# Kernel tuning notes

Measured on AMD Instinct MI355X. Metric: run time of the kernel, lower is better.

## Reference

```python
import jax, jax.numpy as jnp
import numpy as np

D_MODEL, N_HEADS, D_FF = 768, 12, 3072
B, T = 4, 2048
EPS = 1e-5


def setup_inputs() -> dict:
    key = jax.random.key(0)
    ks = jax.random.split(key, 12)
    s = 0.02
    inp = {
        'x': jax.random.normal(ks[0], (B, T, D_MODEL), jnp.float32),
        'mask': jnp.tril(jnp.ones((1, 1, T, T), jnp.bool_)),  # causal decoder mask
        'ln1_g': jnp.ones((D_MODEL,), jnp.float32),
        'ln1_b': jnp.zeros((D_MODEL,), jnp.float32),
        'Wq': jax.random.normal(ks[1], (D_MODEL, D_MODEL), jnp.float32) * s,
        'bq': jnp.zeros((D_MODEL,), jnp.float32),
        'Wk': jax.random.normal(ks[2], (D_MODEL, D_MODEL), jnp.float32) * s,
        'bk': jnp.zeros((D_MODEL,), jnp.float32),
        'Wv': jax.random.normal(ks[3], (D_MODEL, D_MODEL), jnp.float32) * s,
        'bv': jnp.zeros((D_MODEL,), jnp.float32),
        'Wo': jax.random.normal(ks[4], (D_MODEL, D_MODEL), jnp.float32) * s,
        'bo': jnp.zeros((D_MODEL,), jnp.float32),
        'ln2_g': jnp.ones((D_MODEL,), jnp.float32),
        'ln2_b': jnp.zeros((D_MODEL,), jnp.float32),
        'W1': jax.random.normal(ks[5], (D_MODEL, D_FF), jnp.float32) * s,
        'b1': jnp.zeros((D_FF,), jnp.float32),
        'W2': jax.random.normal(ks[6], (D_FF, D_MODEL), jnp.float32) * s,
        'b2': jnp.zeros((D_MODEL,), jnp.float32),
    }
    return inp


def _layer_norm(x, g, b):
    mu = jnp.mean(x, axis=-1, keepdims=True)
    var = jnp.mean(jnp.square(x - mu), axis=-1, keepdims=True)
    return (x - mu) * jax.lax.rsqrt(var + EPS) * g + b


def reference(x, mask, ln1_g, ln1_b, Wq, bq, Wk, bk, Wv, bv, Wo, bo,
              ln2_g, ln2_b, W1, b1, W2, b2):
    Bx, Tx, _ = x.shape
    d_k = D_MODEL // N_HEADS
    # --- attention sublayer (pre-norm) ---
    h = _layer_norm(x, ln1_g, ln1_b)
    q = (h @ Wq + bq).reshape(Bx, Tx, N_HEADS, d_k).transpose(0, 2, 1, 3)
    k = (h @ Wk + bk).reshape(Bx, Tx, N_HEADS, d_k).transpose(0, 2, 1, 3)
    v = (h @ Wv + bv).reshape(Bx, Tx, N_HEADS, d_k).transpose(0, 2, 1, 3)
    scores = jnp.einsum('bhqd,bhkd->bhqk', q, k) / jnp.sqrt(jnp.float32(d_k))
    scores = jnp.where(mask, scores, -jnp.inf)
    weights = jax.nn.softmax(scores, axis=-1)
    attn = jnp.einsum('bhqk,bhkd->bhqd', weights, v)
    attn = attn.transpose(0, 2, 1, 3).reshape(Bx, Tx, D_MODEL)
    x = x + (attn @ Wo + bo)
    # --- FFN sublayer (pre-norm) ---
    h = _layer_norm(x, ln2_g, ln2_b)
    h = jax.nn.gelu(h @ W1 + b1, approximate=False)
    return x + (h @ W2 + b2)
```

## Files before the change

### kernel.cpp

```cpp
#include <hip/hip_runtime.h>

#define DEV __device__ __forceinline__

typedef __attribute__((ext_vector_type(8))) short short8;
typedef __attribute__((ext_vector_type(4))) float f32x4;
typedef __attribute__((ext_vector_type(4))) unsigned int u32x4;
typedef __attribute__((ext_vector_type(2))) unsigned int u32x2;
typedef __attribute__((ext_vector_type(4))) unsigned short u16x4;

constexpr int Bc = 4, Tc = 2048, Dm = 768, Hh = 12, DK = 64, DFF = 3072;
constexpr int MT = Bc * Tc;

DEV unsigned short f2bf(float f) {
  unsigned int u = __float_as_uint(f);
  u += 0x7fff + ((u >> 16) & 1);
  return (unsigned short)(u >> 16);
}

DEV unsigned cvt_pk_bf16(float lo, float hi) {
  unsigned r;
  asm("v_cvt_pk_bf16_f32 %0, %1, %2" : "=v"(r) : "v"(lo), "v"(hi));
  return r;
}

DEV float gelu_fast(float v) {
  float y = 1.5957691216f * (v + 0.044715f * v * v * v);
  return v * (1.0f / (1.0f + __expf(-y)));
}

DEV void gload_lds16(const void* g, void* l) {
  __builtin_amdgcn_global_load_lds(
      (const __attribute__((address_space(1))) void*)g,
      (__attribute__((address_space(3))) void*)l, 16, 0, 0);
}

__global__ __launch_bounds__(256) void ln_kernel(const float* __restrict__ x,
    const float* __restrict__ gam, const float* __restrict__ bet,
    unsigned short* __restrict__ out)
{
  int lane = threadIdx.x & 63;
  int row = blockIdx.x * 4 + (threadIdx.x >> 6);
  const float* xr = x + (size_t)row * Dm + lane * 12;
  f32x4 v0 = *(const f32x4*)(xr);
  f32x4 v1 = *(const f32x4*)(xr + 4);
  f32x4 v2 = *(const f32x4*)(xr + 8);
  float s = 0.f, s2 = 0.f;
#pragma unroll
  for (int j = 0; j < 4; j++) {
    s  += v0[j] + v1[j] + v2[j];
    s2 += v0[j]*v0[j] + v1[j]*v1[j] + v2[j]*v2[j];
  }
#pragma unroll
  for (int off = 32; off; off >>= 1) { s += __shfl_xor(s, off); s2 += __shfl_xor(s2, off); }
  float mu = s * (1.f / Dm);
  float inv = rsqrtf(s2 * (1.f / Dm) - mu * mu + 1e-5f);
  int cb = lane * 12;
  unsigned short o[12];
#pragma unroll
  for (int j = 0; j < 4; j++) {
    o[j]     = f2bf((v0[j] - mu) * inv * gam[cb + j]     + bet[cb + j]);
    o[4 + j] = f2bf((v1[j] - mu) * inv * gam[cb + 4 + j] + bet[cb + 4 + j]);
    o[8 + j] = f2bf((v2[j] - mu) * inv * gam[cb + 8 + j] + bet[cb + 8 + j]);
  }
  unsigned short* orow = out + (size_t)row * Dm + cb;
#pragma unroll
  for (int i = 0; i < 3; i++) *(u16x4*)(orow + i * 4) = *(const u16x4*)(&o[i * 4]);
}

__global__ __launch_bounds__(256) void wtrans_all_kernel(
    const float* __restrict__ Wq, const float* __restrict__ Wk,
    const float* __restrict__ Wv, const float* __restrict__ Wo,
    const float* __restrict__ W1, const float* __restrict__ W2,
    unsigned short* wq_t, unsigned short* wk_t, unsigned short* wv_t,
    unsigned short* wo_t, unsigned short* w1_t, unsigned short* w2_t)
{
  __shared__ unsigned short tile[32][33];
  int bid = blockIdx.x;
  const float* src; unsigned short* dst; int K, N, t;
  if (bid < 2304) {
    int w = bid / 576; t = bid % 576; K = Dm; N = Dm;
    src = w == 0 ? Wq : w == 1 ? Wk : w == 2 ? Wv : Wo;
    dst = w == 0 ? wq_t : w == 1 ? wk_t : w == 2 ? wv_t : wo_t;
  } else if (bid < 4608) {
    t = bid - 2304; K = Dm; N = DFF; src = W1; dst = w1_t;
  } else {
    t = bid - 4608; K = DFF; N = Dm; src = W2; dst = w2_t;
  }
  int gx = N / 32;
  int n0 = (t % gx) * 32, k0 = (t / gx) * 32;
  int tx = threadIdx.x & 31, ty = threadIdx.x >> 5;
#pragma unroll
  for (int i = 0; i < 4; i++) {
    int kr = ty * 4 + i;
    tile[kr][tx] = f2bf(src[(size_t)(k0 + kr) * N + n0 + tx]);
  }
  __syncthreads();
#pragma unroll
  for (int i = 0; i < 4; i++) {
    int nr = ty * 4 + i;
    dst[(size_t)(n0 + nr) * K + k0 + tx] = tile[tx][nr];
  }
}

template<int OUT_MODE, bool SWAP>
DEV void gemm_body(unsigned short* As, unsigned short* Bs,
    const unsigned short* __restrict__ A, const unsigned short* __restrict__ Bt,
    const float* __restrict__ bias, const float* __restrict__ resid, void* __restrict__ out,
    int M, int N, int K)
{
  int m0 = blockIdx.x * 128, n0 = blockIdx.y * 128;
  int tid = threadIdx.x, lane = tid & 63, wid = tid >> 6;
  int wr = wid >> 1, wc = wid & 1;
  int fr = lane & 15, fg = lane >> 4;
  f32x4 acc[4][4] = {};
  for (int k0 = 0; k0 < K; k0 += 64) {
    __syncthreads();
#pragma unroll
    for (int p = 0; p < 4; p++) {
      int L = wid * 256 + p * 64 + lane;
      int row = L >> 3, pos = L & 7;
      int ch = pos ^ (row & 7);
      gload_lds16(&A[(size_t)(m0 + row) * K + k0 + ch * 8],
                  &As[(size_t)(wid * 256 + p * 64) * 8]);
      gload_lds16(&Bt[(size_t)(n0 + row) * K + k0 + ch * 8],
                  &Bs[(size_t)(wid * 256 + p * 64) * 8]);
    }
    __syncthreads();
#pragma unroll
    for (int kk = 0; kk < 2; kk++) {
      short8 af[4], bfr[4];
#pragma unroll
      for (int m = 0; m < 4; m++) {
        int row = wr * 64 + m * 16 + fr;
        int ch = (kk * 4 + fg) ^ (fr & 7);
        af[m] = *(const short8*)(&As[row * 64 + ch * 8]);
      }
#pragma unroll
      for (int n = 0; n < 4; n++) {
        int row = wc * 64 + n * 16 + fr;
        int ch = (kk * 4 + fg) ^ (fr & 7);
        bfr[n] = *(const short8*)(&Bs[row * 64 + ch * 8]);
      }
#pragma unroll
      for (int m = 0; m < 4; m++)
#pragma unroll
        for (int n = 0; n < 4; n++) {
          if (SWAP)
            acc[m][n] = __builtin_amdgcn_mfma_f32_16x16x32_bf16(bfr[n], af[m], acc[m][n], 0, 0, 0);
          else
            acc[m][n] = __builtin_amdgcn_mfma_f32_16x16x32_bf16(af[m], bfr[n], acc[m][n], 0, 0, 0);
        }
    }
  }
  if (SWAP) {
#pragma unroll
    for (int m = 0; m < 4; m++) {
      int gm = m0 + wr * 64 + m * 16 + fr;
#pragma unroll
      for (int n = 0; n < 4; n++) {
        int gn0 = n0 + wc * 64 + n * 16 + fg * 4;
        f32x4 v = acc[m][n];
        f32x4 bv = *(const f32x4*)(bias + gn0);
#pragma unroll
        for (int rr = 0; rr < 4; rr++) v[rr] += bv[rr];
        if (OUT_MODE == 2) {
#pragma unroll
          for (int rr = 0; rr < 4; rr++) v[rr] = gelu_fast(v[rr]);
        }
        if (OUT_MODE == 0) {
          f32x4 rv = *(const f32x4*)(resid + (size_t)gm * N + gn0);
#pragma unroll
          for (int rr = 0; rr < 4; rr++) v[rr] += rv[rr];
          *(f32x4*)(&((float*)out)[(size_t)gm * N + gn0]) = v;
        } else {
          u32x2 pk;
          pk[0] = cvt_pk_bf16(v[0], v[1]);
          pk[1] = cvt_pk_bf16(v[2], v[3]);
          if (OUT_MODE == 3) {
            int b = gm >> 11, tt = gm & 2047, h = gn0 >> 6, d = gn0 & 63;
            *(u32x2*)(&((unsigned short*)out)[(((size_t)b * Hh + h) * Tc + tt) * DK + d]) = pk;
          } else {
            *(u32x2*)(&((unsigned short*)out)[(size_t)gm * N + gn0]) = pk;
          }
        }
      }
    }
  } else {
    int col = fr, rbase = fg * 4;
#pragma unroll
    for (int m = 0; m < 4; m++) {
#pragma unroll
      for (int n = 0; n < 4; n++) {
        int gn = n0 + wc * 64 + n * 16 + col;
        float bv = bias[gn];
        int gm0 = m0 + wr * 64 + m * 16 + rbase;
        int b = gm0 >> 11, tt = gm0 & 2047, h = gn >> 6, d = gn & 63;
        u16x4 pk;
#pragma unroll
        for (int rr = 0; rr < 4; rr++) pk[rr] = f2bf(acc[m][n][rr] + bv);
        *(u16x4*)(&((unsigned short*)out)[(((size_t)b * Hh + h) * DK + d) * Tc + tt]) = pk;
      }
    }
  }
}

__global__ __launch_bounds__(256) void gemm_f32out_kernel(const unsigned short* A,
    const unsigned short* Bt, const float* bias, const float* resid, float* out,
    int M, int N, int K)
{
  __shared__ unsigned short As[128 * 64], Bs[128 * 64];
  gemm_body<0, true>(As, Bs, A, Bt, bias, resid, out, M, N, K);
}

__global__ __launch_bounds__(256) void gemm_gelu_kernel(const unsigned short* A,
    const unsigned short* Bt, const float* bias, unsigned short* out,
    int M, int N, int K)
{
  __shared__ unsigned short As[128 * 64], Bs[128 * 64];
  gemm_body<2, true>(As, Bs, A, Bt, bias, nullptr, out, M, N, K);
}

__global__ __launch_bounds__(256) void gemm_qkv_kernel(const unsigned short* A,
    const unsigned short* Bq, const unsigned short* Bk, const unsigned short* Bv,
    const float* bq, const float* bk, const float* bv,
    unsigned short* oq, unsigned short* okh, unsigned short* ovt)
{
  __shared__ unsigned short As[128 * 64], Bs[128 * 64];
  if (blockIdx.z == 0)      gemm_body<1, true >(As, Bs, A, Bq, bq, nullptr, oq,  MT, Dm, Dm);
  else if (blockIdx.z == 1) gemm_body<3, true >(As, Bs, A, Bk, bk, nullptr, okh, MT, Dm, Dm);
  else                      gemm_body<4, false>(As, Bs, A, Bv, bv, nullptr, ovt, MT, Dm, Dm);
}

__global__ __launch_bounds__(256) void attn_kernel(const unsigned short* __restrict__ q,
    const unsigned short* __restrict__ kh, const unsigned short* __restrict__ vt,
    unsigned short* __restrict__ o)
{
  __shared__ unsigned short Ks[2][64 * 64], Vs[2][64 * 64];
  __shared__ unsigned short P_lds[4][16 * 64];
  int lane = threadIdx.x & 63, wid = threadIdx.x >> 6;
  int fr = lane & 15, fg = lane >> 4;
  int bid = blockIdx.x;
  int xcd = bid & 7, ii = bid >> 3;
  int bh = xcd * 6 + (ii >> 5);
  int qc = 31 - (ii & 31);
  int b = bh / Hh, h = bh - b * Hh;
  int q0 = qc * 64 + wid * 16;
  const size_t qbase = ((size_t)b * Tc) * Dm + h * DK;
  const unsigned short* kg = kh + (size_t)bh * Tc * DK;
  const unsigned short* vg = vt + (size_t)bh * DK * Tc;
  short8 qa0 = *(const short8*)(&q[qbase + (size_t)(q0 + fr) * Dm + fg * 8]);
  short8 qa1 = *(const short8*)(&q[qbase + (size_t)(q0 + fr) * Dm + 32 + fg * 8]);
  f32x4 oa[4] = {};
  f32x4 rs = {};
  short8 onesb;
#pragma unroll
  for (int j = 0; j < 8; j++) onesb[j] = (short)0x3F80;
  unsigned short* Pw = P_lds[wid];
  int nIter = qc + 1;

#define STAGE(buf, kk0)                                                          \
  {                                                                              \
    _Pragma("unroll")                                                            \
    for (int c = 0; c < 2; c++) {                                                \
      int L = c * 256 + wid * 64 + lane;                                         \
      int row = L >> 3, cc = (L & 7) ^ (row & 7);                                \
      gload_lds16(kg + (size_t)((kk0) + row) * DK + cc * 8,                      \
                  &Ks[buf][(size_t)(c * 256 + wid * 64) * 8]);                   \
      gload_lds16(vg + (size_t)row * Tc + (kk0) + cc * 8,                        \
                  &Vs[buf][(size_t)(c * 256 + wid * 64) * 8]);                   \
    }                                                                            \
  }

  STAGE(0, 0)
  for (int it = 0; it < nIter; it++) {
    int cur = it & 1;
    if (it + 1 < nIter) {
      STAGE(cur ^ 1, (it + 1) * 64)
      asm volatile("s_waitcnt vmcnt(4)" ::: "memory");
    } else {
      asm volatile("s_waitcnt vmcnt(0)" ::: "memory");
    }
    __builtin_amdgcn_s_barrier();
    int k0 = it * 64;
    f32x4 st[4];
#pragma unroll
    for (int t = 0; t < 4; t++) {
      int row = t * 16 + fr;
      short8 kf0 = *(const short8*)(&Ks[cur][row * 64 + ((fg)     ^ (fr & 7)) * 8]);
      short8 kf1 = *(const short8*)(&Ks[cur][row * 64 + ((4 + fg) ^ (fr & 7)) * 8]);
      st[t] = {};
      st[t] = __builtin_amdgcn_mfma_f32_16x16x32_bf16(kf0, qa0, st[t], 0, 0, 0);
      st[t] = __builtin_amdgcn_mfma_f32_16x16x32_bf16(kf1, qa1, st[t], 0, 0, 0);
    }
    short8 vb[4][2];
#pragma unroll
    for (int dg = 0; dg < 4; dg++) {
      int row = dg * 16 + fr;
#pragma unroll
      for (int hf = 0; hf < 2; hf++)
        vb[dg][hf] = *(const short8*)(&Vs[cur][row * 64 + ((hf * 4 + fg) ^ (fr & 7)) * 8]);
    }
    bool masked = (it == nIter - 1);
#pragma unroll
    for (int t = 0; t < 4; t++) {
      float p[4];
#pragma unroll
      for (int rr = 0; rr < 4; rr++) {
        float e = __expf(st[t][rr] * 0.125f);
        if (masked) {
          int key = k0 + t * 16 + fg * 4 + rr;
          e = (key <= q0 + fr) ? e : 0.f;
        }
        p[rr] = e;
      }
      u32x2 pkw;
      pkw[0] = cvt_pk_bf16(p[0], p[1]);
      pkw[1] = cvt_pk_bf16(p[2], p[3]);
      int C = t * 2 + (fg >> 1);
      *(u32x2*)(&Pw[fr * 64 + ((C ^ (fr & 7)) << 3) + ((fg & 1) << 2)]) = pkw;
    }
    asm volatile("s_waitcnt lgkmcnt(0)" ::: "memory");
    __builtin_amdgcn_sched_barrier(0);
    short8 pa0 = *(const short8*)(&Pw[fr * 64 + ((fg     ^ (fr & 7)) * 8)]);
    short8 pa1 = *(const short8*)(&Pw[fr * 64 + (((4 + fg) ^ (fr & 7)) * 8)]);
    rs = __builtin_amdgcn_mfma_f32_16x16x32_bf16(pa0, onesb, rs, 0, 0, 0);
    rs = __builtin_amdgcn_mfma_f32_16x16x32_bf16(pa1, onesb, rs, 0, 0, 0);
#pragma unroll
    for (int dg = 0; dg < 4; dg++) {
      oa[dg] = __builtin_amdgcn_mfma_f32_16x16x32_bf16(pa0, vb[dg][0], oa[dg], 0, 0, 0);
      oa[dg] = __builtin_amdgcn_mfma_f32_16x16x32_bf16(pa1, vb[dg][1], oa[dg], 0, 0, 0);
    }
    __builtin_amdgcn_s_barrier();
  }
#undef STAGE
  f32x4 rinv;
#pragma unroll
  for (int rr = 0; rr < 4; rr++) rinv[rr] = __builtin_amdgcn_rcpf(rs[rr]);
#pragma unroll
  for (int dg = 0; dg < 4; dg++)
#pragma unroll
    for (int rr = 0; rr < 4; rr++) {
      int qi = q0 + fg * 4 + rr;
      o[qbase + (size_t)qi * Dm + dg * 16 + fr] = f2bf(oa[dg][rr] * rinv[rr]);
    }
}

extern "C" void kernel_launch(void* const* d_in, const int* in_sizes, int n_in,
                              void* d_out, int out_size, void* d_ws, size_t ws_size,
                              hipStream_t stream) {
  const float* x     = (const float*)d_in[0];
  const float* ln1_g = (const float*)d_in[2];
  const float* ln1_b = (const float*)d_in[3];
  const float* Wq = (const float*)d_in[4];  const float* bq = (const float*)d_in[5];
  const float* Wk = (const float*)d_in[6];  const float* bk = (const float*)d_in[7];
  const float* Wv = (const float*)d_in[8];  const float* bv = (const float*)d_in[9];
  const float* Wo = (const float*)d_in[10]; const float* bo = (const float*)d_in[11];
  const float* ln2_g = (const float*)d_in[12];
  const float* ln2_b = (const float*)d_in[13];
  const float* W1 = (const float*)d_in[14]; const float* b1 = (const float*)d_in[15];
  const float* W2 = (const float*)d_in[16]; const float* b2 = (const float*)d_in[17];
  float* out = (float*)d_out;

  char* ws = (char*)d_ws;
  const size_t HB = (size_t)MT * Dm * 2;
  unsigned short* h_buf  = (unsigned short*)(ws);
  unsigned short* q_buf  = (unsigned short*)(ws + HB);
  unsigned short* kh_buf = (unsigned short*)(ws + 2 * HB);
  unsigned short* vt_buf = (unsigned short*)(ws + 3 * HB);
  unsigned short* wq_t   = (unsigned short*)(ws + 4 * HB);
  unsigned short* wk_t   = wq_t + (size_t)Dm * Dm;
  unsigned short* wv_t   = wk_t + (size_t)Dm * Dm;
  unsigned short* wo_t   = wv_t + (size_t)Dm * Dm;
  unsigned short* w1_t   = wo_t + (size_t)Dm * Dm;
  unsigned short* w2_t   = w1_t + (size_t)Dm * DFF;
  unsigned short* g_buf  = w2_t + (size_t)DFF * Dm;

  wtrans_all_kernel<<<dim3(6912), 256, 0, stream>>>(
      Wq, Wk, Wv, Wo, W1, W2, wq_t, wk_t, wv_t, wo_t, w1_t, w2_t);

  ln_kernel<<<MT / 4, 256, 0, stream>>>(x, ln1_g, ln1_b, h_buf);
  gemm_qkv_kernel<<<dim3(MT / 128, Dm / 128, 3), 256, 0, stream>>>(
      h_buf, wq_t, wk_t, wv_t, bq, bk, bv, q_buf, kh_buf, vt_buf);
  attn_kernel<<<dim3(1536), 256, 0, stream>>>(q_buf, kh_buf, vt_buf, h_buf);
  gemm_f32out_kernel<<<dim3(MT / 128, Dm / 128), 256, 0, stream>>>(
      h_buf, wo_t, bo, x, out, MT, Dm, Dm);
  ln_kernel<<<MT / 4, 256, 0, stream>>>(out, ln2_g, ln2_b, h_buf);
  gemm_gelu_kernel<<<dim3(MT / 128, DFF / 128), 256, 0, stream>>>(
      h_buf, w1_t, b1, g_buf, MT, DFF, Dm);
  gemm_f32out_kernel<<<dim3(MT / 128, Dm / 128), 256, 0, stream>>>(
      g_buf, w2_t, b2, out, out, MT, Dm, DFF);
}
```

Measured before the change: 276.8 us.

## Switch GEMM to 32x32x16 MFMA tiles and hoist load address math

The GEMM inner loop moves from sixteen 16x16x32 MFMA accumulators per wave to four 32x32x16 accumulators. This halves the LDS fragment reads per MFMA and changes the epilogue to match the 32x32 output layout. Per-lane global and LDS load addresses are now computed once, outside the K loop in the GEMM and outside the KV loop in attention. The risks are higher accumulator register pressure and a harder epilogue mapping, which must be correct for every output mode.

```diff
diff --git a/kernel.cpp b/kernel.cpp
--- a/kernel.cpp
+++ b/kernel.cpp
@@ -4,6 +4,7 @@
 
 typedef __attribute__((ext_vector_type(8))) short short8;
 typedef __attribute__((ext_vector_type(4))) float f32x4;
+typedef __attribute__((ext_vector_type(16))) float f32x16;
 typedef __attribute__((ext_vector_type(4))) unsigned int u32x4;
 typedef __attribute__((ext_vector_type(2))) unsigned int u32x2;
 typedef __attribute__((ext_vector_type(4))) unsigned short u16x4;
@@ -111,94 +112,105 @@
   int m0 = blockIdx.x * 128, n0 = blockIdx.y * 128;
   int tid = threadIdx.x, lane = tid & 63, wid = tid >> 6;
   int wr = wid >> 1, wc = wid & 1;
-  int fr = lane & 15, fg = lane >> 4;
-  f32x4 acc[4][4] = {};
+  int r32 = lane & 31, l5 = lane >> 5;
+  const unsigned short* pA[4]; const unsigned short* pB[4];
+  unsigned short* dA[4]; unsigned short* dB[4];
+#pragma unroll
+  for (int p = 0; p < 4; p++) {
+    int L = wid * 256 + p * 64 + lane;
+    int row = L >> 3, pos = L & 7;
+    int ch = pos ^ (row & 7);
+    pA[p] = A + (size_t)(m0 + row) * K + ch * 8;
+    pB[p] = Bt + (size_t)(n0 + row) * K + ch * 8;
+    dA[p] = As + (size_t)L * 8;
+    dB[p] = Bs + (size_t)L * 8;
+  }
+  f32x16 acc[2][2] = {};
   for (int k0 = 0; k0 < K; k0 += 64) {
     __syncthreads();
 #pragma unroll
     for (int p = 0; p < 4; p++) {
-      int L = wid * 256 + p * 64 + lane;
-      int row = L >> 3, pos = L & 7;
-      int ch = pos ^ (row & 7);
-      gload_lds16(&A[(size_t)(m0 + row) * K + k0 + ch * 8],
-                  &As[(size_t)(wid * 256 + p * 64) * 8]);
-      gload_lds16(&Bt[(size_t)(n0 + row) * K + k0 + ch * 8],
-                  &Bs[(size_t)(wid * 256 + p * 64) * 8]);
+      gload_lds16(pA[p] + k0, dA[p]);
+      gload_lds16(pB[p] + k0, dB[p]);
     }
     __syncthreads();
 #pragma unroll
-    for (int kk = 0; kk < 2; kk++) {
-      short8 af[4], bfr[4];
-#pragma unroll
-      for (int m = 0; m < 4; m++) {
-        int row = wr * 64 + m * 16 + fr;
-        int ch = (kk * 4 + fg) ^ (fr & 7);
-        af[m] = *(const short8*)(&As[row * 64 + ch * 8]);
+    for (int kk = 0; kk < 4; kk++) {
+      short8 af[2], bfr[2];
+#pragma unroll
+      for (int g = 0; g < 2; g++) {
+        int rowA = wr * 64 + g * 32 + r32;
+        af[g]  = *(const short8*)(&As[rowA * 64 + (((kk * 2 + l5) ^ (rowA & 7)) << 3)]);
+        int rowB = wc * 64 + g * 32 + r32;
+        bfr[g] = *(const short8*)(&Bs[rowB * 64 + (((kk * 2 + l5) ^ (rowB & 7)) << 3)]);
       }
 #pragma unroll
-      for (int n = 0; n < 4; n++) {
-        int row = wc * 64 + n * 16 + fr;
-        int ch = (kk * 4 + fg) ^ (fr & 7);
-        bfr[n] = *(const short8*)(&Bs[row * 64 + ch * 8]);
-      }
-#pragma unroll
-      for (int m = 0; m < 4; m++)
-#pragma unroll
-        for (int n = 0; n < 4; n++) {
+      for (int mg = 0; mg < 2; mg++)
+#pragma unroll
+        for (int ng = 0; ng < 2; ng++) {
           if (SWAP)
-            acc[m][n] = __builtin_amdgcn_mfma_f32_16x16x32_bf16(bfr[n], af[m], acc[m][n], 0, 0, 0);
+            acc[mg][ng] = __builtin_amdgcn_mfma_f32_32x32x16_bf16(bfr[ng], af[mg], acc[mg][ng], 0, 0, 0);
           else
-            acc[m][n] = __builtin_amdgcn_mfma_f32_16x16x32_bf16(af[m], bfr[n], acc[m][n], 0, 0, 0);
+            acc[mg][ng] = __builtin_amdgcn_mfma_f32_32x32x16_bf16(af[mg], bfr[ng], acc[mg][ng], 0, 0, 0);
         }
     }
   }
   if (SWAP) {
 #pragma unroll
-    for (int m = 0; m < 4; m++) {
-      int gm = m0 + wr * 64 + m * 16 + fr;
-#pragma unroll
-      for (int n = 0; n < 4; n++) {
-        int gn0 = n0 + wc * 64 + n * 16 + fg * 4;
-        f32x4 v = acc[m][n];
-        f32x4 bv = *(const f32x4*)(bias + gn0);
-#pragma unroll
-        for (int rr = 0; rr < 4; rr++) v[rr] += bv[rr];
-        if (OUT_MODE == 2) {
-#pragma unroll
-          for (int rr = 0; rr < 4; rr++) v[rr] = gelu_fast(v[rr]);
-        }
-        if (OUT_MODE == 0) {
-          f32x4 rv = *(const f32x4*)(resid + (size_t)gm * N + gn0);
-#pragma unroll
-          for (int rr = 0; rr < 4; rr++) v[rr] += rv[rr];
-          *(f32x4*)(&((float*)out)[(size_t)gm * N + gn0]) = v;
-        } else {
-          u32x2 pk;
-          pk[0] = cvt_pk_bf16(v[0], v[1]);
-          pk[1] = cvt_pk_bf16(v[2], v[3]);
-          if (OUT_MODE == 3) {
-            int b = gm >> 11, tt = gm & 2047, h = gn0 >> 6, d = gn0 & 63;
-            *(u32x2*)(&((unsigned short*)out)[(((size_t)b * Hh + h) * Tc + tt) * DK + d]) = pk;
+    for (int mg = 0; mg < 2; mg++) {
+      int gm = m0 + wr * 64 + mg * 32 + r32;
+#pragma unroll
+      for (int ng = 0; ng < 2; ng++) {
+        int nbase = n0 + wc * 64 + ng * 32;
+#pragma unroll
+        for (int rq = 0; rq < 4; rq++) {
+          int gn0 = nbase + rq * 8 + l5 * 4;
+          f32x4 v;
+#pragma unroll
+          for (int rr = 0; rr < 4; rr++) v[rr] = acc[mg][ng][rq * 4 + rr];
+          f32x4 bv = *(const f32x4*)(bias + gn0);
+#pragma unroll
+          for (int rr = 0; rr < 4; rr++) v[rr] += bv[rr];
+          if (OUT_MODE == 2) {
+#pragma unroll
+            for (int rr = 0; rr < 4; rr++) v[rr] = gelu_fast(v[rr]);
+          }
+          if (OUT_MODE == 0) {
+            f32x4 rv = *(const f32x4*)(resid + (size_t)gm * N + gn0);
+#pragma unroll
+            for (int rr = 0; rr < 4; rr++) v[rr] += rv[rr];
+            *(f32x4*)(&((float*)out)[(size_t)gm * N + gn0]) = v;
           } else {
-            *(u32x2*)(&((unsigned short*)out)[(size_t)gm * N + gn0]) = pk;
+            u32x2 pk;
+            pk[0] = cvt_pk_bf16(v[0], v[1]);
+            pk[1] = cvt_pk_bf16(v[2], v[3]);
+            if (OUT_MODE == 3) {
+              int b = gm >> 11, tt = gm & 2047, h = gn0 >> 6, d = gn0 & 63;
+              *(u32x2*)(&((unsigned short*)out)[(((size_t)b * Hh + h) * Tc + tt) * DK + d]) = pk;
+            } else {
+              *(u32x2*)(&((unsigned short*)out)[(size_t)gm * N + gn0]) = pk;
+            }
           }
         }
       }
     }
   } else {
-    int col = fr, rbase = fg * 4;
-#pragma unroll
-    for (int m = 0; m < 4; m++) {
-#pragma unroll
-      for (int n = 0; n < 4; n++) {
-        int gn = n0 + wc * 64 + n * 16 + col;
+#pragma unroll
+    for (int mg = 0; mg < 2; mg++) {
+#pragma unroll
+      for (int ng = 0; ng < 2; ng++) {
+        int gn = n0 + wc * 64 + ng * 32 + r32;
         float bv = bias[gn];
-        int gm0 = m0 + wr * 64 + m * 16 + rbase;
-        int b = gm0 >> 11, tt = gm0 & 2047, h = gn >> 6, d = gn & 63;
-        u16x4 pk;
-#pragma unroll
-        for (int rr = 0; rr < 4; rr++) pk[rr] = f2bf(acc[m][n][rr] + bv);
-        *(u16x4*)(&((unsigned short*)out)[(((size_t)b * Hh + h) * DK + d) * Tc + tt]) = pk;
+        int h = gn >> 6, d = gn & 63;
+#pragma unroll
+        for (int rq = 0; rq < 4; rq++) {
+          int gm0 = m0 + wr * 64 + mg * 32 + rq * 8 + l5 * 4;
+          int b = gm0 >> 11, tt = gm0 & 2047;
+          u16x4 pk;
+#pragma unroll
+          for (int rr = 0; rr < 4; rr++) pk[rr] = f2bf(acc[mg][ng][rq * 4 + rr] + bv);
+          *(u16x4*)(&((unsigned short*)out)[(((size_t)b * Hh + h) * DK + d) * Tc + tt]) = pk;
+        }
       }
     }
   }
@@ -248,6 +260,16 @@
   const size_t qbase = ((size_t)b * Tc) * Dm + h * DK;
   const unsigned short* kg = kh + (size_t)bh * Tc * DK;
   const unsigned short* vg = vt + (size_t)bh * DK * Tc;
+  const unsigned short* pK[2]; const unsigned short* pV[2];
+  int ldsoff[2];
+#pragma unroll
+  for (int c = 0; c < 2; c++) {
+    int L = c * 256 + wid * 64 + lane;
+    int row = L >> 3, cc = (L & 7) ^ (row & 7);
+    pK[c] = kg + (size_t)row * DK + cc * 8;
+    pV[c] = vg + (size_t)row * Tc + cc * 8;
+    ldsoff[c] = L * 8;
+  }
   short8 qa0 = *(const short8*)(&q[qbase + (size_t)(q0 + fr) * Dm + fg * 8]);
   short8 qa1 = *(const short8*)(&q[qbase + (size_t)(q0 + fr) * Dm + 32 + fg * 8]);
   f32x4 oa[4] = {};
@@ -262,12 +284,8 @@
   {                                                                              \
     _Pragma("unroll")                                                            \
     for (int c = 0; c < 2; c++) {                                                \
-      int L = c * 256 + wid * 64 + lane;                                         \
-      int row = L >> 3, cc = (L & 7) ^ (row & 7);                                \
-      gload_lds16(kg + (size_t)((kk0) + row) * DK + cc * 8,                      \
-                  &Ks[buf][(size_t)(c * 256 + wid * 64) * 8]);                   \
-      gload_lds16(vg + (size_t)row * Tc + (kk0) + cc * 8,                        \
-                  &Vs[buf][(size_t)(c * 256 + wid * 64) * 8]);                   \
+      gload_lds16(pK[c] + (size_t)(kk0) * DK, &Ks[buf][ldsoff[c]]);              \
+      gload_lds16(pV[c] + (kk0),              &Vs[buf][ldsoff[c]]);              \
     }                                                                            \
   }
 
```

After: 272.0 us. No clear change (-1.7%).
